# Kernel optimization log

Hardware: AMD Instinct MI355X
Metric: run time of the kernel (lower is better)

## Reference

```python
import jax, jax.numpy as jnp
import numpy as np

E, D, I, TOPK, N = 8, 2048, 4096, 2, 4096


def setup_inputs() -> dict:
    key = jax.random.key(0)
    k_x, k_w, k_i, k_g, k_u, k_d = jax.random.split(key, 6)
    x = jax.random.normal(k_x, (N, D), dtype=jnp.float32)
    expert_weights = jax.random.uniform(k_w, (N, TOPK), dtype=jnp.float32)
    expert_indices = jax.random.randint(k_i, (N, TOPK), 0, E).astype(jnp.int32)
    s_in = np.float32(1.0 / np.sqrt(D))
    s_mid = np.float32(1.0 / np.sqrt(I))
    # SwitchLinear weights: [num_experts, out_features, in_features]
    wg = jax.random.normal(k_g, (E, I, D), dtype=jnp.float32) * s_in
    wu = jax.random.normal(k_u, (E, I, D), dtype=jnp.float32) * s_in
    wd = jax.random.normal(k_d, (E, D, I), dtype=jnp.float32) * s_mid
    return {"x": x, "expert_weights": expert_weights,
            "expert_indices": expert_indices, "top_k": TOPK,
            "wg": wg, "wu": wu, "wd": wd}


def reference(x, expert_weights, expert_indices, top_k, wg, wu, wd):
    # out[n] = sum_k expert_weights[n,k] * Wd[e] @ (silu(Wg[e] x[n]) * (Wu[e] x[n]))
    #          with e = expert_indices[n,k].
    # Grouped-by-expert form (identical math): accumulate each expert's
    # contribution over all tokens, weighted by its routing weight (0 if not routed).
    num_experts = wg.shape[0]
    out = jnp.zeros_like(x)
    for e in range(num_experts):
        # per-token routing weight for expert e (sums over top_k slots)
        w_e = jnp.sum(jnp.where(expert_indices == e, expert_weights, 0.0), axis=-1)  # [N]
        gate = x @ wg[e].T            # [N, I]
        up = x @ wu[e].T              # [N, I]
        h = jax.nn.silu(gate) * up    # SwiGLU, [N, I]
        out = out + w_e[:, None] * (h @ wd[e].T)  # [N, D]
    return out
```

## Files before the change

### kernel.cpp

```cpp
#include <hip/hip_runtime.h>
#include <hip/hip_bf16.h>
#include <math.h>

#define E_ 8
#define D_ 2048
#define I_ 4096
#define TOPK_ 2
#define N_ 4096
#define NPAIR (N_*TOPK_)
#define PADMAX 10240
#define MAXTB256 40
#define NIB 16
#define CVTX 13
#define CH_X   (1L<<20)
#define CH_HALF (1L<<22)
#define CH_WD  (1L<<23)

typedef __attribute__((ext_vector_type(8))) short s8v;
typedef __attribute__((ext_vector_type(8))) unsigned short us8;
typedef __attribute__((ext_vector_type(4))) float f32x4;
typedef const __attribute__((address_space(1))) void* gvp;
typedef __attribute__((address_space(3))) void* lvp;

__device__ __forceinline__ unsigned short f2bf(float f) {
  union { float f; unsigned int u; } c; c.f = f;
  unsigned int u = c.u;
  u += 0x7fffu + ((u >> 16) & 1u);
  return (unsigned short)(u >> 16);
}

__device__ __forceinline__ void cvt_chunk(const float* __restrict__ src,
                                          unsigned short* __restrict__ dst,
                                          size_t off) {
  float4 a = *(const float4*)(src + off);
  float4 b = *(const float4*)(src + off + 4);
  us8 o;
  o[0]=f2bf(a.x); o[1]=f2bf(a.y); o[2]=f2bf(a.z); o[3]=f2bf(a.w);
  o[4]=f2bf(b.x); o[5]=f2bf(b.y); o[6]=f2bf(b.z); o[7]=f2bf(b.w);
  *(us8*)(dst + off) = o;
}

__device__ __forceinline__ void cvt_half(const float* __restrict__ src,
                                         unsigned short* __restrict__ dst,
                                         long chunk, int ihalf) {
  long f = chunk << 3;
  int e = (int)(f >> 22);
  long r = f & ((1L << 22) - 1);
  size_t off = ((size_t)e << 23) + ((size_t)ihalf << 22) + (size_t)r;
  cvt_chunk(src, dst, off);
}

__global__ __launch_bounds__(512)
void head_kernel(const int* __restrict__ idx, const float* __restrict__ ew,
                 int* cnt, int* offs, int* tb, int* ntb,
                 int* perm, float* wgt,
                 const float* __restrict__ x, unsigned short* __restrict__ xb,
                 const float* __restrict__ wg, unsigned short* __restrict__ wgb,
                 const float* __restrict__ wu, unsigned short* __restrict__ wub)
{
  if (blockIdx.x == 0) {
    __shared__ int scnt[E_], soff[E_ + 1], scur[E_];
    int t = threadIdx.x;
    if (t < E_) scnt[t] = 0;
    __syncthreads();
    for (int p = t; p < NPAIR; p += blockDim.x) atomicAdd(&scnt[idx[p]], 1);
    __syncthreads();
    if (t == 0) {
      int o = 0;
      for (int e = 0; e < E_; e++) {
        soff[e] = o; scur[e] = o;
        o += ((scnt[e] + 255) / 256) * 256;
      }
      soff[E_] = o;
      int T = 0;
      for (int e = 0; e < E_; e++) {
        int nb = (scnt[e] + 255) / 256;
        for (int rb = 0; rb < nb; rb++) tb[T++] = (e << 16) | rb;
      }
      *ntb = T;
      for (int e = 0; e < E_; e++) { cnt[e] = scnt[e]; offs[e] = soff[e]; }
      offs[E_] = o;
    }
    __syncthreads();
    for (int e = 0; e < E_; e++) {
      int start = soff[e] + scnt[e], end = soff[e + 1];
      for (int s = start + t; s < end; s += blockDim.x) { perm[s] = -1; wgt[s] = 0.f; }
    }
    __syncthreads();
    for (int p = t; p < NPAIR; p += blockDim.x) {
      int e = idx[p];
      int pos = atomicAdd(&scur[e], 1);
      perm[pos] = p / TOPK_;
      wgt[pos]  = ew[p];
    }
    return;
  }
  const long TOTAL = CH_X + 2 * CH_HALF;
  long c0 = (long)(blockIdx.x - 1) * 512 + threadIdx.x;
  long stride = (long)(gridDim.x - 1) * 512;
  for (long c = c0; c < TOTAL; c += stride) {
    if (c < CH_X) cvt_chunk(x, xb, (size_t)c << 3);
    else if (c < CH_X + CH_HALF) cvt_half(wg, wgb, c - CH_X, 0);
    else cvt_half(wu, wub, c - CH_X - CH_HALF, 0);
  }
}

#define A_SLAB(P,KH) (((P)*2+(KH))*8192)
#define B_SLAB(P,KH) (32768 + ((P)*2+(KH))*8192)

#define SB  __builtin_amdgcn_sched_barrier(0)
#define BARR __builtin_amdgcn_s_barrier()
#define VMW(N) asm volatile("s_waitcnt vmcnt(" #N ")" ::: "memory")
#define LGK asm volatile("s_waitcnt lgkmcnt(0)" ::: "memory")
#define PRIO1 __builtin_amdgcn_s_setprio(1)
#define PRIO0 __builtin_amdgcn_s_setprio(0)

#define LOAD_A(P,KH,MH) { \
  const unsigned short* ap_ = &smem[A_SLAB(P,KH) + aBase + (MH)*2048]; \
  af[0] = *(const s8v*)(ap_);      af[1] = *(const s8v*)(ap_+512); \
  af[2] = *(const s8v*)(ap_+1024); af[3] = *(const s8v*)(ap_+1536); }

#define LOAD_B(P,KH) { \
  const unsigned short* bp_ = &smem[B_SLAB(P,KH) + bBase]; \
  bf[0] = *(const s8v*)(bp_);      bf[1] = *(const s8v*)(bp_+512); \
  bf[2] = *(const s8v*)(bp_+1024); bf[3] = *(const s8v*)(bp_+1536); }

#define STAGE_A(T,KH,P) { \
  __builtin_amdgcn_global_load_lds((gvp)(aptr0 + (T)*64 + (KH)*32), (lvp)(&smem[A_SLAB(P,KH) + (w*2+0)*512]), 16, 0, 0); \
  __builtin_amdgcn_global_load_lds((gvp)(aptr1 + (T)*64 + (KH)*32), (lvp)(&smem[A_SLAB(P,KH) + (w*2+1)*512]), 16, 0, 0); }

#define STAGE_B(T,KH,P) { \
  __builtin_amdgcn_global_load_lds((gvp)(bptr0 + (T)*64 + (KH)*32), (lvp)(&smem[B_SLAB(P,KH) + (w*2+0)*512]), 16, 0, 0); \
  __builtin_amdgcn_global_load_lds((gvp)(bptr1 + (T)*64 + (KH)*32), (lvp)(&smem[B_SLAB(P,KH) + (w*2+1)*512]), 16, 0, 0); }

#define MFMA16(MH) { \
  _Pragma("unroll") for (int m_ = 0; m_ < 4; m_++) \
    _Pragma("unroll") for (int n_ = 0; n_ < 4; n_++) \
      acc[(MH)*4+m_][n_] = __builtin_amdgcn_mfma_f32_16x16x32_bf16(af[m_], bf[n_], acc[(MH)*4+m_][n_], 0, 0, 0); }

#define TILE_PHASES(T, P, Pn, NT_) { \
  if (T) { VMW(4); SB; } \
  LOAD_B(P, 0); LOAD_A(P, 0, 0); \
  if ((T) + 1 < (NT_)) { STAGE_A((T)+1, 1, Pn); } \
  SB; BARR; LGK; SB; \
  PRIO1; MFMA16(0); PRIO0; SB; BARR; SB; \
  LOAD_A(P, 0, 1); \
  if ((T) + 1 < (NT_)) { STAGE_B((T)+1, 1, Pn); } \
  SB; BARR; LGK; SB; \
  PRIO1; MFMA16(1); PRIO0; SB; BARR; SB; \
  if ((T) == (NT_) - 1) { VMW(0); SB; } else { VMW(4); SB; } \
  LOAD_B(P, 1); LOAD_A(P, 1, 0); \
  if ((T) + 2 < (NT_)) { STAGE_A((T)+2, 0, P); } \
  SB; BARR; LGK; SB; \
  PRIO1; MFMA16(0); PRIO0; SB; BARR; SB; \
  LOAD_A(P, 1, 1); \
  if ((T) + 2 < (NT_)) { STAGE_B((T)+2, 0, P); } \
  SB; BARR; LGK; SB; \
  PRIO1; MFMA16(1); PRIO0; SB; BARR; SB; }

#define K_LOOP(NT_) { \
  STAGE_A(0,0,0); STAGE_B(0,0,0); STAGE_A(0,1,0); STAGE_B(0,1,0); \
  STAGE_A(1,0,1); STAGE_B(1,0,1); \
  VMW(8); SB; BARR; SB; \
  _Pragma("unroll 1") \
  for (int tt = 0; tt < (NT_)/2; ++tt) { \
    TILE_PHASES(2*tt,   0, 1, NT_); \
    TILE_PHASES(2*tt+1, 1, 0, NT_); \
  } }

__global__ __launch_bounds__(512, 2)
void gu8_kernel(const unsigned short* __restrict__ xb,
                const unsigned short* __restrict__ wgb,
                const unsigned short* __restrict__ wub,
                const int* __restrict__ tb, const int* __restrict__ ntb,
                const int* __restrict__ offs, const int* __restrict__ perm,
                unsigned short* __restrict__ H,
                int i_base, int cvt_mode,
                const float* __restrict__ cs0, unsigned short* __restrict__ cd0,
                const float* __restrict__ cs1, unsigned short* __restrict__ cd1)
{
  __shared__ unsigned short smem[65536];

  if (blockIdx.x >= MAXTB256) {
    long cid = (long)(blockIdx.x - MAXTB256) + (long)CVTX * blockIdx.y;
    long c0 = cid * 512 + threadIdx.x;
    long stride = (long)CVTX * NIB * 512;
    if (cvt_mode == 1) {
      for (long c = c0; c < 2 * CH_HALF; c += stride) {
        if (c < CH_HALF) cvt_half(cs0, cd0, c, 1);
        else cvt_half(cs1, cd1, c - CH_HALF, 1);
      }
    } else {
      for (long c = c0; c < CH_WD; c += stride) cvt_chunk(cs0, cd0, (size_t)c << 3);
    }
    return;
  }

  int lid = blockIdx.y * MAXTB256 + blockIdx.x;
  int sid = (lid & 7) * (MAXTB256 * NIB / 8) + (lid >> 3);
  int bx = sid % MAXTB256;
  int by = sid / MAXTB256;
  if (bx >= *ntb) return;
  int ent = tb[bx];
  int e = ent >> 16, rb = ent & 0xffff;
  int slotbase = offs[e] + rb * 256;
  int i0 = i_base + by * 128;

  int tid = threadIdx.x, lane = tid & 63, w = tid >> 6;
  int wr = w >> 2, wc = w & 3;

  int cS = (lane & 7) ^ (lane >> 3);
  int rrS = 2 * (lane >> 3) + (cS >> 2);
  int kcS = (cS & 3) * 8;
  int ar0 = (w * 2 + 0) * 16 + rrS;
  int tk0 = perm[slotbase + ar0];       if (tk0 < 0) tk0 = 0;
  int tk1 = perm[slotbase + ar0 + 16];  if (tk1 < 0) tk1 = 0;
  const unsigned short* aptr0 = xb + (size_t)tk0 * D_ + kcS;
  const unsigned short* aptr1 = xb + (size_t)tk1 * D_ + kcS;
  const unsigned short* bptr0 = wgb + ((size_t)e * I_ + i0 + w * 16 + rrS) * D_ + kcS;
  const unsigned short* bptr1 = wub + ((size_t)e * I_ + i0 + w * 16 + rrS) * D_ + kcS;

  int hl = (lane & 15) >> 1;
  int pA = (((lane & 1) * 4 + (lane >> 4)) ^ hl) * 8;
  int aBase = wr * 4096 + hl * 64 + pA;
  int bBase = wc * 2048 + hl * 64 + pA;

  s8v af[4], bf[4];
  f32x4 acc[8][4];
#pragma unroll
  for (int m = 0; m < 8; m++)
#pragma unroll
    for (int n = 0; n < 4; n++) acc[m][n] = f32x4{0.f,0.f,0.f,0.f};

  K_LOOP(32);

#pragma unroll
  for (int m = 0; m < 8; m++) {
#pragma unroll
    for (int r = 0; r < 4; r++) {
      int row = wr * 128 + m * 16 + (lane >> 4) * 4 + r;
      size_t hbase = (size_t)(slotbase + row) * I_ + i0 + (lane & 15);
#pragma unroll
      for (int pr = 0; pr < 2; pr++) {
        float g = acc[m][pr*2][r];
        float u = acc[m][pr*2+1][r];
        float h = (g / (1.0f + __expf(-g))) * u;
        H[hbase + (wc * 2 + pr) * 16] = f2bf(h);
      }
    }
  }
}

__global__ __launch_bounds__(512, 2)
void down8_kernel(const unsigned short* __restrict__ H,
                  const unsigned short* __restrict__ wdb,
                  const int* __restrict__ tb, const int* __restrict__ ntb,
                  const int* __restrict__ offs, const int* __restrict__ perm,
                  const float* __restrict__ wgt,
                  float* __restrict__ out)
{
  __shared__ unsigned short smem[65536];

  int nwg = gridDim.x * gridDim.y * gridDim.z;
  int lid = (blockIdx.z * gridDim.y + blockIdx.y) * gridDim.x + blockIdx.x;
  int cpx = nwg >> 3;
  int sid = (lid & 7) * cpx + (lid >> 3);
  int bx = sid % gridDim.x;
  int rem = sid / gridDim.x;
  int by = rem % gridDim.y;
  int z  = rem / gridDim.y;
  if (bx >= *ntb) return;
  int ent = tb[bx];
  int e = ent >> 16, rb = ent & 0xffff;
  int slotbase = offs[e] + rb * 256;
  int d0 = by * 256;
  int kb = z * (I_ / 2);

  int tid = threadIdx.x, lane = tid & 63, w = tid >> 6;
  int wr = w >> 2, wc = w & 3;

  int cS = (lane & 7) ^ (lane >> 3);
  int rrS = 2 * (lane >> 3) + (cS >> 2);
  int kcS = (cS & 3) * 8;
  int ar0 = (w * 2 + 0) * 16 + rrS;
  const unsigned short* aptr0 = H + (size_t)(slotbase + ar0) * I_ + kcS + kb;
  const unsigned short* aptr1 = H + (size_t)(slotbase + ar0 + 16) * I_ + kcS + kb;
  const unsigned short* bptr0 = wdb + ((size_t)e * D_ + d0 + (w*2+0)*16 + rrS) * I_ + kcS + kb;
  const unsigned short* bptr1 = wdb + ((size_t)e * D_ + d0 + (w*2+1)*16 + rrS) * I_ + kcS + kb;

  int hl = (lane & 15) >> 1;
  int pA = (((lane & 1) * 4 + (lane >> 4)) ^ hl) * 8;
  int aBase = wr * 4096 + hl * 64 + pA;
  int bBase = wc * 2048 + hl * 64 + pA;

  s8v af[4], bf[4];
  f32x4 acc[8][4];
#pragma unroll
  for (int m = 0; m < 8; m++)
#pragma unroll
    for (int n = 0; n < 4; n++) acc[m][n] = f32x4{0.f,0.f,0.f,0.f};

  K_LOOP(32);

#pragma unroll
  for (int m = 0; m < 8; m++) {
#pragma unroll
    for (int r = 0; r < 4; r++) {
      int row = wr * 128 + m * 16 + (lane >> 4) * 4 + r;
      int s = slotbase + row;
      int tok = perm[s];
      if (tok < 0) continue;
      float wv = wgt[s];
      float* op = out + (size_t)tok * D_ + d0 + wc * 64 + (lane & 15);
#pragma unroll
      for (int n = 0; n < 4; n++)
        atomicAdd(op + n * 16, acc[m][n][r] * wv);
    }
  }
}

extern "C" void kernel_launch(void* const* d_in, const int* in_sizes, int n_in,
                              void* d_out, int out_size, void* d_ws, size_t ws_size,
                              hipStream_t stream)
{
  const float* x  = (const float*)d_in[0];
  const float* ew = (const float*)d_in[1];
  const int*  idx = (const int*)d_in[2];
  const float* wg = (const float*)d_in[4];
  const float* wu = (const float*)d_in[5];
  const float* wd = (const float*)d_in[6];
  float* out = (float*)d_out;

  char* ws = (char*)d_ws;
  int* cnt   = (int*)(ws);
  int* ntb   = (int*)(ws + 64);
  int* tb    = (int*)(ws + 128);
  int* offs  = (int*)(ws + 640);
  int* perm  = (int*)(ws + 4096);
  float* wgt = (float*)(ws + 4096 + PADMAX * 4);

  const size_t xb_off = 131072;
  const size_t xb_b   = (size_t)N_ * D_ * 2;
  const size_t H_b    = (size_t)PADMAX * I_ * 2;
  const size_t w_b    = (size_t)E_ * I_ * D_ * 2;
  unsigned short* xb  = (unsigned short*)(ws + xb_off);
  unsigned short* H   = (unsigned short*)(ws + xb_off + xb_b);
  unsigned short* wgb = (unsigned short*)(ws + xb_off + xb_b + H_b);
  unsigned short* wub = (unsigned short*)((char*)wgb + w_b);
  unsigned short* wdb = (unsigned short*)((char*)wub + w_b);

  hipMemsetAsync(d_out, 0, (size_t)N_ * D_ * sizeof(float), stream);
  head_kernel<<<2048, 512, 0, stream>>>(idx, ew, cnt, offs, tb, ntb, perm, wgt,
                                        x, xb, wg, wgb, wu, wub);
  gu8_kernel<<<dim3(MAXTB256 + CVTX, NIB), 512, 0, stream>>>(
      xb, wgb, wub, tb, ntb, offs, perm, H, 0, 1, wg, wgb, wu, wub);
  gu8_kernel<<<dim3(MAXTB256 + CVTX, NIB), 512, 0, stream>>>(
      xb, wgb, wub, tb, ntb, offs, perm, H, I_ / 2, 2, wd, wdb, (const float*)0, (unsigned short*)0);
  down8_kernel<<<dim3(MAXTB256, D_ / 256, 2), 512, 0, stream>>>(
      H, wdb, tb, ntb, offs, perm, wgt, out);
}
```

Before: 837.9 us.

## Replace down-proj atomic scatter with bf16 staging plus gather; load A fragments once

The down-projection kernel now writes bf16 partial results (one per K-half) into a slot-indexed scratch buffer that reuses the wg bf16 region, instead of doing weighted fp32 atomicAdds into the output. A new gather kernel sums the two K-halves and the two top-k slots per token using a token-to-slot map recorded in the head kernel, which also removes the output memset. Separately, the MFMA loop loads all eight A fragments at once, removing one barrier and LDS wait per half-tile at the cost of extra registers. The bf16 rounding of partial sums adds some precision loss.

```diff
diff --git a/kernel.cpp b/kernel.cpp
--- a/kernel.cpp
+++ b/kernel.cpp
@@ -28,6 +28,9 @@
   u += 0x7fffu + ((u >> 16) & 1u);
   return (unsigned short)(u >> 16);
 }
+__device__ __forceinline__ float bf2f(unsigned short u) {
+  return __uint_as_float(((unsigned int)u) << 16);
+}
 
 __device__ __forceinline__ void cvt_chunk(const float* __restrict__ src,
                                           unsigned short* __restrict__ dst,
@@ -53,7 +56,7 @@
 __global__ __launch_bounds__(512)
 void head_kernel(const int* __restrict__ idx, const float* __restrict__ ew,
                  int* cnt, int* offs, int* tb, int* ntb,
-                 int* perm, float* wgt,
+                 int* perm, float* wgt, int* ts,
                  const float* __restrict__ x, unsigned short* __restrict__ xb,
                  const float* __restrict__ wg, unsigned short* __restrict__ wgb,
                  const float* __restrict__ wu, unsigned short* __restrict__ wub)
@@ -92,6 +95,7 @@
       int pos = atomicAdd(&scur[e], 1);
       perm[pos] = p / TOPK_;
       wgt[pos]  = ew[p];
+      ts[p]     = pos;
     }
     return;
   }
@@ -115,10 +119,12 @@
 #define PRIO1 __builtin_amdgcn_s_setprio(1)
 #define PRIO0 __builtin_amdgcn_s_setprio(0)
 
-#define LOAD_A(P,KH,MH) { \
-  const unsigned short* ap_ = &smem[A_SLAB(P,KH) + aBase + (MH)*2048]; \
+#define LOAD_A8(P,KH) { \
+  const unsigned short* ap_ = &smem[A_SLAB(P,KH) + aBase]; \
   af[0] = *(const s8v*)(ap_);      af[1] = *(const s8v*)(ap_+512); \
-  af[2] = *(const s8v*)(ap_+1024); af[3] = *(const s8v*)(ap_+1536); }
+  af[2] = *(const s8v*)(ap_+1024); af[3] = *(const s8v*)(ap_+1536); \
+  af[4] = *(const s8v*)(ap_+2048); af[5] = *(const s8v*)(ap_+2560); \
+  af[6] = *(const s8v*)(ap_+3072); af[7] = *(const s8v*)(ap_+3584); }
 
 #define LOAD_B(P,KH) { \
   const unsigned short* bp_ = &smem[B_SLAB(P,KH) + bBase]; \
@@ -136,27 +142,23 @@
 #define MFMA16(MH) { \
   _Pragma("unroll") for (int m_ = 0; m_ < 4; m_++) \
     _Pragma("unroll") for (int n_ = 0; n_ < 4; n_++) \
-      acc[(MH)*4+m_][n_] = __builtin_amdgcn_mfma_f32_16x16x32_bf16(af[m_], bf[n_], acc[(MH)*4+m_][n_], 0, 0, 0); }
+      acc[(MH)*4+m_][n_] = __builtin_amdgcn_mfma_f32_16x16x32_bf16(af[(MH)*4+m_], bf[n_], acc[(MH)*4+m_][n_], 0, 0, 0); }
 
 #define TILE_PHASES(T, P, Pn, NT_) { \
   if (T) { VMW(4); SB; } \
-  LOAD_B(P, 0); LOAD_A(P, 0, 0); \
+  LOAD_B(P, 0); LOAD_A8(P, 0); \
   if ((T) + 1 < (NT_)) { STAGE_A((T)+1, 1, Pn); } \
   SB; BARR; LGK; SB; \
   PRIO1; MFMA16(0); PRIO0; SB; BARR; SB; \
-  LOAD_A(P, 0, 1); \
   if ((T) + 1 < (NT_)) { STAGE_B((T)+1, 1, Pn); } \
-  SB; BARR; LGK; SB; \
-  PRIO1; MFMA16(1); PRIO0; SB; BARR; SB; \
+  SB; PRIO1; MFMA16(1); PRIO0; SB; BARR; SB; \
   if ((T) == (NT_) - 1) { VMW(0); SB; } else { VMW(4); SB; } \
-  LOAD_B(P, 1); LOAD_A(P, 1, 0); \
+  LOAD_B(P, 1); LOAD_A8(P, 1); \
   if ((T) + 2 < (NT_)) { STAGE_A((T)+2, 0, P); } \
   SB; BARR; LGK; SB; \
   PRIO1; MFMA16(0); PRIO0; SB; BARR; SB; \
-  LOAD_A(P, 1, 1); \
   if ((T) + 2 < (NT_)) { STAGE_B((T)+2, 0, P); } \
-  SB; BARR; LGK; SB; \
-  PRIO1; MFMA16(1); PRIO0; SB; BARR; SB; }
+  SB; PRIO1; MFMA16(1); PRIO0; SB; BARR; SB; }
 
 #define K_LOOP(NT_) { \
   STAGE_A(0,0,0); STAGE_B(0,0,0); STAGE_A(0,1,0); STAGE_B(0,1,0); \
@@ -225,7 +227,7 @@
   int aBase = wr * 4096 + hl * 64 + pA;
   int bBase = wc * 2048 + hl * 64 + pA;
 
-  s8v af[4], bf[4];
+  s8v af[8], bf[4];
   f32x4 acc[8][4];
 #pragma unroll
   for (int m = 0; m < 8; m++)
@@ -256,8 +258,7 @@
                   const unsigned short* __restrict__ wdb,
                   const int* __restrict__ tb, const int* __restrict__ ntb,
                   const int* __restrict__ offs, const int* __restrict__ perm,
-                  const float* __restrict__ wgt,
-                  float* __restrict__ out)
+                  unsigned short* __restrict__ C)
 {
   __shared__ unsigned short smem[65536];
 
@@ -293,7 +294,7 @@
   int aBase = wr * 4096 + hl * 64 + pA;
   int bBase = wc * 2048 + hl * 64 + pA;
 
-  s8v af[4], bf[4];
+  s8v af[8], bf[4];
   f32x4 acc[8][4];
 #pragma unroll
   for (int m = 0; m < 8; m++)
@@ -302,21 +303,46 @@
 
   K_LOOP(32);
 
+  unsigned short* cb = C + ((size_t)z * PADMAX + slotbase) * (size_t)D_ + d0 + wc * 64 + (lane & 15);
 #pragma unroll
   for (int m = 0; m < 8; m++) {
 #pragma unroll
     for (int r = 0; r < 4; r++) {
       int row = wr * 128 + m * 16 + (lane >> 4) * 4 + r;
-      int s = slotbase + row;
-      int tok = perm[s];
-      if (tok < 0) continue;
-      float wv = wgt[s];
-      float* op = out + (size_t)tok * D_ + d0 + wc * 64 + (lane & 15);
+      unsigned short* cp = cb + (size_t)row * D_;
 #pragma unroll
       for (int n = 0; n < 4; n++)
-        atomicAdd(op + n * 16, acc[m][n][r] * wv);
-    }
-  }
+        cp[n * 16] = f2bf(acc[m][n][r]);
+    }
+  }
+}
+
+__global__ __launch_bounds__(256)
+void gather_kernel(const unsigned short* __restrict__ C,
+                   const int* __restrict__ ts, const float* __restrict__ wgt,
+                   float* __restrict__ out)
+{
+  int n = blockIdx.x;
+  int dc = threadIdx.x;
+  int s0 = ts[2 * n], s1 = ts[2 * n + 1];
+  float w0 = wgt[s0], w1 = wgt[s1];
+  size_t dof = (size_t)dc * 8;
+  us8 a = *(const us8*)(C + ((size_t)s0) * D_ + dof);
+  us8 b = *(const us8*)(C + ((size_t)s1) * D_ + dof);
+  us8 c = *(const us8*)(C + ((size_t)PADMAX + s0) * D_ + dof);
+  us8 d = *(const us8*)(C + ((size_t)PADMAX + s1) * D_ + dof);
+  float4 o0, o1;
+  o0.x = w0*(bf2f(a[0])+bf2f(c[0])) + w1*(bf2f(b[0])+bf2f(d[0]));
+  o0.y = w0*(bf2f(a[1])+bf2f(c[1])) + w1*(bf2f(b[1])+bf2f(d[1]));
+  o0.z = w0*(bf2f(a[2])+bf2f(c[2])) + w1*(bf2f(b[2])+bf2f(d[2]));
+  o0.w = w0*(bf2f(a[3])+bf2f(c[3])) + w1*(bf2f(b[3])+bf2f(d[3]));
+  o1.x = w0*(bf2f(a[4])+bf2f(c[4])) + w1*(bf2f(b[4])+bf2f(d[4]));
+  o1.y = w0*(bf2f(a[5])+bf2f(c[5])) + w1*(bf2f(b[5])+bf2f(d[5]));
+  o1.z = w0*(bf2f(a[6])+bf2f(c[6])) + w1*(bf2f(b[6])+bf2f(d[6]));
+  o1.w = w0*(bf2f(a[7])+bf2f(c[7])) + w1*(bf2f(b[7])+bf2f(d[7]));
+  float* op = out + (size_t)n * D_ + dof;
+  *(float4*)(op)     = o0;
+  *(float4*)(op + 4) = o1;
 }
 
 extern "C" void kernel_launch(void* const* d_in, const int* in_sizes, int n_in,
@@ -338,6 +364,7 @@
   int* offs  = (int*)(ws + 640);
   int* perm  = (int*)(ws + 4096);
   float* wgt = (float*)(ws + 4096 + PADMAX * 4);
+  int* ts    = (int*)(ws + 4096 + 2 * PADMAX * 4);
 
   const size_t xb_off = 131072;
   const size_t xb_b   = (size_t)N_ * D_ * 2;
@@ -348,14 +375,15 @@
   unsigned short* wgb = (unsigned short*)(ws + xb_off + xb_b + H_b);
   unsigned short* wub = (unsigned short*)((char*)wgb + w_b);
   unsigned short* wdb = (unsigned short*)((char*)wub + w_b);
-
-  hipMemsetAsync(d_out, 0, (size_t)N_ * D_ * sizeof(float), stream);
-  head_kernel<<<2048, 512, 0, stream>>>(idx, ew, cnt, offs, tb, ntb, perm, wgt,
+  unsigned short* C   = wgb;
+
+  head_kernel<<<2048, 512, 0, stream>>>(idx, ew, cnt, offs, tb, ntb, perm, wgt, ts,
                                         x, xb, wg, wgb, wu, wub);
   gu8_kernel<<<dim3(MAXTB256 + CVTX, NIB), 512, 0, stream>>>(
       xb, wgb, wub, tb, ntb, offs, perm, H, 0, 1, wg, wgb, wu, wub);
   gu8_kernel<<<dim3(MAXTB256 + CVTX, NIB), 512, 0, stream>>>(
       xb, wgb, wub, tb, ntb, offs, perm, H, I_ / 2, 2, wd, wdb, (const float*)0, (unsigned short*)0);
   down8_kernel<<<dim3(MAXTB256, D_ / 256, 2), 512, 0, stream>>>(
-      H, wdb, tb, ntb, offs, perm, wgt, out);
-}
+      H, wdb, tb, ntb, offs, perm, C);
+  gather_kernel<<<N_, 256, 0, stream>>>(C, ts, wgt, out);
+}
```

Measured after the change: 886.3 us. 5.8% more time.

## Read fp32 down-proj weights directly, converting to bf16 in LDS-to-register path

Applied to the files above, without the earlier changes.

Removes the separate fp32→bf16 conversion pass for the down-projection weights, which the second gate/up launch used to run in spare blocks. The down kernel now streams fp32 Wd into shared memory and converts to bf16 when loading fragments. To make room, its output tile width is halved to 128 columns, with twice as many column blocks. This trades an extra write and read of a converted weight copy for twice the fp32 bytes per B tile, per-fragment conversion ALU work, and more re-reads of the H tiles across the doubled grid.

```diff
diff --git a/kernel.cpp b/kernel.cpp
--- a/kernel.cpp
+++ b/kernel.cpp
@@ -11,10 +11,9 @@
 #define PADMAX 10240
 #define MAXTB256 40
 #define NIB 16
-#define CVTX 13
+#define CVTX 16
 #define CH_X   (1L<<20)
 #define CH_HALF (1L<<22)
-#define CH_WD  (1L<<23)
 
 typedef __attribute__((ext_vector_type(8))) short s8v;
 typedef __attribute__((ext_vector_type(8))) unsigned short us8;
@@ -190,8 +189,6 @@
         if (c < CH_HALF) cvt_half(cs0, cd0, c, 1);
         else cvt_half(cs1, cd1, c - CH_HALF, 1);
       }
-    } else {
-      for (long c = c0; c < CH_WD; c += stride) cvt_chunk(cs0, cd0, (size_t)c << 3);
     }
     return;
   }
@@ -251,9 +248,60 @@
   }
 }
 
+#define STAGE_B32(T,KH,P) { \
+  __builtin_amdgcn_global_load_lds((gvp)(bptr0 + (T)*64 + (KH)*32), (lvp)(&smem[B_SLAB(P,KH) + 0*4096 + w*512]), 16, 0, 0); \
+  __builtin_amdgcn_global_load_lds((gvp)(bptr1 + (T)*64 + (KH)*32), (lvp)(&smem[B_SLAB(P,KH) + 1*4096 + w*512]), 16, 0, 0); }
+
+#define LOAD_B32(P,KH) { \
+  const float* fb_ = (const float*)&smem[B_SLAB(P,KH)]; \
+  _Pragma("unroll") for (int n_ = 0; n_ < 2; n_++) { \
+    int r_ = wc * 32 + n_ * 16 + (lane & 15); \
+    int s_ = r_ & 7; int ks_ = (lane >> 4) * 2; \
+    float4 u_ = *(const float4*)(fb_ + r_ * 32 + ((ks_    ) ^ s_) * 4); \
+    float4 v_ = *(const float4*)(fb_ + r_ * 32 + ((ks_ + 1) ^ s_) * 4); \
+    s8v t_; \
+    t_[0]=(short)f2bf(u_.x); t_[1]=(short)f2bf(u_.y); t_[2]=(short)f2bf(u_.z); t_[3]=(short)f2bf(u_.w); \
+    t_[4]=(short)f2bf(v_.x); t_[5]=(short)f2bf(v_.y); t_[6]=(short)f2bf(v_.z); t_[7]=(short)f2bf(v_.w); \
+    bf[n_] = t_; } }
+
+#define MFMA8(MH) { \
+  _Pragma("unroll") for (int m_ = 0; m_ < 4; m_++) \
+    _Pragma("unroll") for (int n_ = 0; n_ < 2; n_++) \
+      acc[(MH)*4+m_][n_] = __builtin_amdgcn_mfma_f32_16x16x32_bf16(af[m_], bf[n_], acc[(MH)*4+m_][n_], 0, 0, 0); }
+
+#define TILE_PHASES32(T, P, Pn, NT_) { \
+  if (T) { VMW(4); SB; } \
+  LOAD_B32(P, 0); LOAD_A(P, 0, 0); \
+  if ((T) + 1 < (NT_)) { STAGE_A((T)+1, 1, Pn); } \
+  SB; BARR; LGK; SB; \
+  PRIO1; MFMA8(0); PRIO0; SB; BARR; SB; \
+  LOAD_A(P, 0, 1); \
+  if ((T) + 1 < (NT_)) { STAGE_B32((T)+1, 1, Pn); } \
+  SB; BARR; LGK; SB; \
+  PRIO1; MFMA8(1); PRIO0; SB; BARR; SB; \
+  if ((T) == (NT_) - 1) { VMW(0); SB; } else { VMW(4); SB; } \
+  LOAD_B32(P, 1); LOAD_A(P, 1, 0); \
+  if ((T) + 2 < (NT_)) { STAGE_A((T)+2, 0, P); } \
+  SB; BARR; LGK; SB; \
+  PRIO1; MFMA8(0); PRIO0; SB; BARR; SB; \
+  LOAD_A(P, 1, 1); \
+  if ((T) + 2 < (NT_)) { STAGE_B32((T)+2, 0, P); } \
+  SB; BARR; LGK; SB; \
+  PRIO1; MFMA8(1); PRIO0; SB; BARR; SB; }
+
+#define K_LOOP32(NT_) { \
+  STAGE_A(0,0,0); STAGE_B32(0,0,0); STAGE_A(0,1,0); STAGE_B32(0,1,0); \
+  STAGE_A(1,0,1); STAGE_B32(1,0,1); \
+  VMW(8); SB; BARR; SB; \
+  _Pragma("unroll 1") \
+  for (int tt = 0; tt < (NT_)/2; ++tt) { \
+    TILE_PHASES32(2*tt,   0, 1, NT_); \
+    TILE_PHASES32(2*tt+1, 1, 0, NT_); \
+  } }
+
 __global__ __launch_bounds__(512, 2)
 void down8_kernel(const unsigned short* __restrict__ H,
-                  const unsigned short* __restrict__ wdb,
+                  const float* __restrict__ wd,
                   const int* __restrict__ tb, const int* __restrict__ ntb,
                   const int* __restrict__ offs, const int* __restrict__ perm,
                   const float* __restrict__ wgt,
@@ -261,19 +309,17 @@
 {
   __shared__ unsigned short smem[65536];
 
-  int nwg = gridDim.x * gridDim.y * gridDim.z;
   int lid = (blockIdx.z * gridDim.y + blockIdx.y) * gridDim.x + blockIdx.x;
-  int cpx = nwg >> 3;
-  int sid = (lid & 7) * cpx + (lid >> 3);
-  int bx = sid % gridDim.x;
-  int rem = sid / gridDim.x;
-  int by = rem % gridDim.y;
-  int z  = rem / gridDim.y;
+  int sid = (lid & 7) * 160 + (lid >> 3);
+  int bx = sid % MAXTB256;
+  int rem = sid / MAXTB256;
+  int by = rem & 15;
+  int z  = rem >> 4;
   if (bx >= *ntb) return;
   int ent = tb[bx];
   int e = ent >> 16, rb = ent & 0xffff;
   int slotbase = offs[e] + rb * 256;
-  int d0 = by * 256;
+  int d0 = by * 128;
   int kb = z * (I_ / 2);
 
   int tid = threadIdx.x, lane = tid & 63, w = tid >> 6;
@@ -285,22 +331,23 @@
   int ar0 = (w * 2 + 0) * 16 + rrS;
   const unsigned short* aptr0 = H + (size_t)(slotbase + ar0) * I_ + kcS + kb;
   const unsigned short* aptr1 = H + (size_t)(slotbase + ar0 + 16) * I_ + kcS + kb;
-  const unsigned short* bptr0 = wdb + ((size_t)e * D_ + d0 + (w*2+0)*16 + rrS) * I_ + kcS + kb;
-  const unsigned short* bptr1 = wdb + ((size_t)e * D_ + d0 + (w*2+1)*16 + rrS) * I_ + kcS + kb;
+  int rowS = w * 8 + (lane >> 3);
+  int kfS = ((lane & 7) ^ (lane >> 3)) * 4;
+  const float* bptr0 = wd + ((size_t)e * D_ + d0 + rowS) * I_ + kb + kfS;
+  const float* bptr1 = wd + ((size_t)e * D_ + d0 + rowS + 64) * I_ + kb + kfS;
 
   int hl = (lane & 15) >> 1;
   int pA = (((lane & 1) * 4 + (lane >> 4)) ^ hl) * 8;
   int aBase = wr * 4096 + hl * 64 + pA;
-  int bBase = wc * 2048 + hl * 64 + pA;
-
-  s8v af[4], bf[4];
-  f32x4 acc[8][4];
+
+  s8v af[4], bf[2];
+  f32x4 acc[8][2];
 #pragma unroll
   for (int m = 0; m < 8; m++)
 #pragma unroll
-    for (int n = 0; n < 4; n++) acc[m][n] = f32x4{0.f,0.f,0.f,0.f};
-
-  K_LOOP(32);
+    for (int n = 0; n < 2; n++) acc[m][n] = f32x4{0.f,0.f,0.f,0.f};
+
+  K_LOOP32(32);
 
 #pragma unroll
   for (int m = 0; m < 8; m++) {
@@ -311,9 +358,9 @@
       int tok = perm[s];
       if (tok < 0) continue;
       float wv = wgt[s];
-      float* op = out + (size_t)tok * D_ + d0 + wc * 64 + (lane & 15);
-#pragma unroll
-      for (int n = 0; n < 4; n++)
+      float* op = out + (size_t)tok * D_ + d0 + wc * 32 + (lane & 15);
+#pragma unroll
+      for (int n = 0; n < 2; n++)
         atomicAdd(op + n * 16, acc[m][n][r] * wv);
     }
   }
@@ -347,15 +394,15 @@
   unsigned short* H   = (unsigned short*)(ws + xb_off + xb_b);
   unsigned short* wgb = (unsigned short*)(ws + xb_off + xb_b + H_b);
   unsigned short* wub = (unsigned short*)((char*)wgb + w_b);
-  unsigned short* wdb = (unsigned short*)((char*)wub + w_b);
 
   hipMemsetAsync(d_out, 0, (size_t)N_ * D_ * sizeof(float), stream);
   head_kernel<<<2048, 512, 0, stream>>>(idx, ew, cnt, offs, tb, ntb, perm, wgt,
                                         x, xb, wg, wgb, wu, wub);
   gu8_kernel<<<dim3(MAXTB256 + CVTX, NIB), 512, 0, stream>>>(
       xb, wgb, wub, tb, ntb, offs, perm, H, 0, 1, wg, wgb, wu, wub);
-  gu8_kernel<<<dim3(MAXTB256 + CVTX, NIB), 512, 0, stream>>>(
-      xb, wgb, wub, tb, ntb, offs, perm, H, I_ / 2, 2, wd, wdb, (const float*)0, (unsigned short*)0);
-  down8_kernel<<<dim3(MAXTB256, D_ / 256, 2), 512, 0, stream>>>(
-      H, wdb, tb, ntb, offs, perm, wgt, out);
-}
+  gu8_kernel<<<dim3(MAXTB256, NIB), 512, 0, stream>>>(
+      xb, wgb, wub, tb, ntb, offs, perm, H, I_ / 2, 0,
+      (const float*)0, (unsigned short*)0, (const float*)0, (unsigned short*)0);
+  down8_kernel<<<dim3(MAXTB256, 16, 2), 512, 0, stream>>>(
+      H, wd, tb, ntb, offs, perm, wgt, out);
+}
```

Measured after the change: 938.0 us. 1.12x slower.
